# Optimization experiments

Measured on AMD Instinct MI355X. Metric: run time of the kernel, lower is better.

The kernel has to match this reference:

```python
import jax, jax.numpy as jnp
import numpy as np

# nuScenes-style config: 6 cams, 4 FPN levels of a 256x704 image
SPATIAL = np.array([[64, 176], [32, 88], [16, 44], [8, 22]], dtype=np.int32)  # (H, W) per level
NUM_CAMS = 6
EMBED = 256      # embed dims C
GROUPS = 8       # attention groups, C % GROUPS == 0
BS = 2
ANCHORS = 900    # queries
PTS = 13         # key points per anchor


def setup_inputs() -> dict:
    key = jax.random.key(0)
    k1, k2, k3 = jax.random.split(key, 3)
    hw = SPATIAL.prod(axis=1)                                   # per-level H*W
    starts = np.concatenate([[0], np.cumsum(hw)[:-1]]).astype(np.int32)
    num_value = NUM_CAMS * int(hw.sum())                        # 6 * 14960 = 89760
    value = jax.random.normal(k1, (BS, num_value, EMBED), jnp.float32)
    input_spatial_shapes = jnp.asarray(np.tile(SPATIAL[None], (NUM_CAMS, 1, 1)))   # [cams, lvls, 2]
    input_level_start_index = jnp.asarray(np.tile(starts[None], (NUM_CAMS, 1)))    # [cams, lvls]
    sampling_locations = jax.random.uniform(k2, (BS, ANCHORS, PTS, NUM_CAMS, 2), jnp.float32)
    attention_weights = jax.random.uniform(k3, (BS, ANCHORS, PTS, NUM_CAMS, SPATIAL.shape[0], GROUPS), jnp.float32)
    return {
        "value": value,
        "input_spatial_shapes": input_spatial_shapes,
        "input_level_start_index": input_level_start_index,
        "sampling_locations": sampling_locations,
        "attention_weights": attention_weights,
    }


def _dfa(value, shapes, starts, loc, weights):
    """Multi-scale multi-camera deformable aggregation (Sparse4D kernel math)."""
    bs, num_value, c = value.shape
    num_cams, num_levels = shapes.shape[:2]
    _, A, P = loc.shape[:3]
    groups = weights.shape[-1]
    gdim = c // groups
    per_cam = num_value // num_cams
    value_c = value.reshape(bs, num_cams, per_cam, c)           # cam-major layout
    b_idx = jnp.arange(bs)[:, None, None, None]
    cam_idx = jnp.arange(num_cams)[None, None, None, :]
    loc_w = loc[..., 0]                                          # [bs, A, P, cams]
    loc_h = loc[..., 1]
    out = jnp.zeros((bs, A, groups, gdim), value.dtype)
    for lvl in range(num_levels):                                # static small loop over levels
        H = int(shapes[0, lvl, 0]); W = int(shapes[0, lvl, 1]); s = int(starts[0, lvl])
        featf = value_c[:, :, s:s + H * W, :]                    # [bs, cams, H*W, c]
        h = loc_h * H - 0.5
        w = loc_w * W - 0.5
        h0 = jnp.floor(h); w0 = jnp.floor(w)
        dh = h - h0; dw = w - w0
        h0i = h0.astype(jnp.int32); w0i = w0.astype(jnp.int32)

        def corner(hi, wi, bw):
            valid = (hi >= 0) & (hi < H) & (wi >= 0) & (wi < W)  # zero padding outside
            idx = jnp.clip(hi, 0, H - 1) * W + jnp.clip(wi, 0, W - 1)
            v = featf[b_idx, cam_idx, idx]                       # gather -> [bs, A, P, cams, c]
            return v * (bw * valid)[..., None]

        samp = (corner(h0i,     w0i,     (1 - dh) * (1 - dw))
              + corner(h0i,     w0i + 1, (1 - dh) * dw)
              + corner(h0i + 1, w0i,     dh * (1 - dw))
              + corner(h0i + 1, w0i + 1, dh * dw))               # bilinear sample [bs, A, P, cams, c]
        samp = samp.reshape(bs, A, P, num_cams, groups, gdim)
        out = out + jnp.einsum("bapcgd,bapcg->bagd", samp, weights[..., lvl, :])
    return out.reshape(bs, A, c)


def reference(value, input_spatial_shapes, input_level_start_index, sampling_locations, attention_weights):
    shapes = np.asarray(input_spatial_shapes)
    starts = np.asarray(input_level_start_index)
    return _dfa(value, shapes, starts, sampling_locations, attention_weights)
```

## Files before the change

kernel.cpp:

```cpp
#include <hip/hip_runtime.h>

constexpr int NCAMS   = 6;
constexpr int EMB     = 256;
constexpr int NGROUPS = 8;
constexpr int NLVL    = 4;
constexpr int NPTS    = 13;
constexpr int NPAIR   = NPTS * NCAMS;

__global__ __launch_bounds__(256, 4)
void dfa_kernel(const float* __restrict__ value,
                const int*   __restrict__ shapes,
                const int*   __restrict__ starts,
                const float* __restrict__ loc,
                const float* __restrict__ attw,
                float*       __restrict__ out,
                int A, int per_cam)
{
    const int tid  = threadIdx.x;
    const int wv   = tid >> 6;
    const int lane = tid & 63;
    const int b = blockIdx.x / A;
    const int a = blockIdx.x - b * A;

    __shared__ int   sH[NLVL], sW[NLVL], sS[NLVL];
    __shared__ float red[4][EMB];
    if (tid < NLVL) {
        sH[tid] = shapes[tid * 2 + 0];
        sW[tid] = shapes[tid * 2 + 1];
        sS[tid] = starts[tid];
    }
    __syncthreads();

    const int g = lane >> 3;
    const long ba = (long)b * A + a;
    const float* locp = loc  + ba * (NPTS * NCAMS * 2);
    const float* awp  = attw + ba * (NPTS * NCAMS * NLVL * NGROUPS) + g;

    float4 acc = make_float4(0.f, 0.f, 0.f, 0.f);

    for (int pair = wv; pair < NPAIR; pair += 4) {
        const int p = pair / NCAMS;
        const int c = pair - p * NCAMS;
        const float lw = locp[pair * 2 + 0];
        const float lh = locp[pair * 2 + 1];
        const float* vb = value + ((long)(b * NCAMS + c) * per_cam) * EMB + lane * 4;
        const float* awpc = awp + pair * (NLVL * NGROUPS);

        #pragma unroll
        for (int lvl = 0; lvl < NLVL; ++lvl) {
            const int H = sH[lvl], W = sW[lvl], S = sS[lvl];
            const float hf = lh * (float)H - 0.5f;
            const float wf = lw * (float)W - 0.5f;
            const float h0f = floorf(hf), w0f = floorf(wf);
            const float dh = hf - h0f, dw = wf - w0f;
            const int h0 = (int)h0f, w0 = (int)w0f;
            const int h1 = h0 + 1,  w1 = w0 + 1;

            const float aw = awpc[lvl * NGROUPS];

            float w00 = (1.f - dh) * (1.f - dw) * aw;
            float w01 = (1.f - dh) * dw         * aw;
            float w10 = dh         * (1.f - dw) * aw;
            float w11 = dh         * dw         * aw;

            const bool vh0 = (unsigned)h0 < (unsigned)H;
            const bool vh1 = (unsigned)h1 < (unsigned)H;
            const bool vw0 = (unsigned)w0 < (unsigned)W;
            const bool vw1 = (unsigned)w1 < (unsigned)W;
            w00 = (vh0 && vw0) ? w00 : 0.f;
            w01 = (vh0 && vw1) ? w01 : 0.f;
            w10 = (vh1 && vw0) ? w10 : 0.f;
            w11 = (vh1 && vw1) ? w11 : 0.f;

            const int h0c = min(max(h0, 0), H - 1);
            const int h1c = min(max(h1, 0), H - 1);
            const int w0c = min(max(w0, 0), W - 1);
            const int w1c = min(max(w1, 0), W - 1);

            const float* r0 = vb + (long)(S + h0c * W) * EMB;
            const float* r1 = vb + (long)(S + h1c * W) * EMB;

            const float4 v00 = *(const float4*)(r0 + (long)w0c * EMB);
            const float4 v01 = *(const float4*)(r0 + (long)w1c * EMB);
            const float4 v10 = *(const float4*)(r1 + (long)w0c * EMB);
            const float4 v11 = *(const float4*)(r1 + (long)w1c * EMB);

            acc.x += v00.x * w00 + v01.x * w01 + v10.x * w10 + v11.x * w11;
            acc.y += v00.y * w00 + v01.y * w01 + v10.y * w10 + v11.y * w11;
            acc.z += v00.z * w00 + v01.z * w01 + v10.z * w10 + v11.z * w11;
            acc.w += v00.w * w00 + v01.w * w01 + v10.w * w10 + v11.w * w11;
        }
    }

    *(float4*)&red[wv][lane * 4] = acc;
    __syncthreads();

    const float o = red[0][tid] + red[1][tid] + red[2][tid] + red[3][tid];
    out[ba * EMB + tid] = o;
}

extern "C" void kernel_launch(void* const* d_in, const int* in_sizes, int n_in,
                              void* d_out, int out_size, void* d_ws, size_t ws_size,
                              hipStream_t stream) {
    const float* value  = (const float*)d_in[0];
    const int*   shapes = (const int*)d_in[1];
    const int*   starts = (const int*)d_in[2];
    const float* loc    = (const float*)d_in[3];
    const float* attw   = (const float*)d_in[4];
    float*       out    = (float*)d_out;

    const int B = 2;
    const int A = out_size / (EMB * B);
    const int per_cam = in_sizes[0] / (B * EMB * NCAMS);

    dim3 grid(B * A);
    dim3 block(256);
    dfa_kernel<<<grid, block, 0, stream>>>(value, shapes, starts, loc, attw, out,
                                           A, per_cam);
}
```

Measured before the change: 466.5 us.

## Split per-anchor sampling pairs across extra grid dimension with partial-sum reduction

Splits each anchor's point-camera pairs across four blocks along a new grid dimension. The partial sums are written to workspace and combined by a separate reduction kernel, with an atomic fallback when workspace is too small. The aim is more independent blocks and outstanding gathers, and less tail imbalance from the long per-wave loop. In exchange it adds an extra kernel launch, workspace traffic and repeated per-block setup.

```diff
diff --git a/kernel.cpp b/kernel.cpp
--- a/kernel.cpp
+++ b/kernel.cpp
@@ -6,19 +6,22 @@
 constexpr int NLVL    = 4;
 constexpr int NPTS    = 13;
 constexpr int NPAIR   = NPTS * NCAMS;
+constexpr int SPLIT   = 4;
 
+template <bool USE_ATOMIC>
 __global__ __launch_bounds__(256, 4)
 void dfa_kernel(const float* __restrict__ value,
                 const int*   __restrict__ shapes,
                 const int*   __restrict__ starts,
                 const float* __restrict__ loc,
                 const float* __restrict__ attw,
-                float*       __restrict__ out,
+                float*       __restrict__ dst,
                 int A, int per_cam)
 {
-    const int tid  = threadIdx.x;
-    const int wv   = tid >> 6;
-    const int lane = tid & 63;
+    const int tid   = threadIdx.x;
+    const int wv    = tid >> 6;
+    const int lane  = tid & 63;
+    const int split = blockIdx.y;
     const int b = blockIdx.x / A;
     const int a = blockIdx.x - b * A;
 
@@ -38,7 +41,7 @@
 
     float4 acc = make_float4(0.f, 0.f, 0.f, 0.f);
 
-    for (int pair = wv; pair < NPAIR; pair += 4) {
+    for (int pair = wv + (split << 2); pair < NPAIR; pair += 4 * SPLIT) {
         const int p = pair / NCAMS;
         const int c = pair - p * NCAMS;
         const float lw = locp[pair * 2 + 0];
@@ -96,7 +99,32 @@
     __syncthreads();
 
     const float o = red[0][tid] + red[1][tid] + red[2][tid] + red[3][tid];
-    out[ba * EMB + tid] = o;
+    if (USE_ATOMIC) {
+        atomicAdd(&dst[ba * EMB + tid], o);
+    } else {
+        dst[((long)split * gridDim.x + ba) * EMB + tid] = o;
+    }
+}
+
+__global__ __launch_bounds__(256, 4)
+void reduce_kernel(const float* __restrict__ ws, float* __restrict__ out, int n4)
+{
+    const int i = blockIdx.x * blockDim.x + threadIdx.x;
+    if (i >= n4) return;
+    const float4* p = (const float4*)ws;
+    float4 s = p[i];
+    #pragma unroll
+    for (int sp = 1; sp < SPLIT; ++sp) {
+        const float4 q = p[(long)sp * n4 + i];
+        s.x += q.x; s.y += q.y; s.z += q.z; s.w += q.w;
+    }
+    ((float4*)out)[i] = s;
+}
+
+__global__ void zero_kernel(float* __restrict__ out, int n4)
+{
+    const int i = blockIdx.x * blockDim.x + threadIdx.x;
+    if (i < n4) ((float4*)out)[i] = make_float4(0.f, 0.f, 0.f, 0.f);
 }
 
 extern "C" void kernel_launch(void* const* d_in, const int* in_sizes, int n_in,
@@ -112,9 +140,22 @@
     const int B = 2;
     const int A = out_size / (EMB * B);
     const int per_cam = in_sizes[0] / (B * EMB * NCAMS);
+    const int BA = B * A;
+    const size_t need = (size_t)SPLIT * BA * EMB * sizeof(float);
 
-    dim3 grid(B * A);
+    dim3 grid(BA, SPLIT);
     dim3 block(256);
-    dfa_kernel<<<grid, block, 0, stream>>>(value, shapes, starts, loc, attw, out,
-                                           A, per_cam);
+
+    if (ws_size >= need) {
+        float* ws = (float*)d_ws;
+        dfa_kernel<false><<<grid, block, 0, stream>>>(value, shapes, starts, loc,
+                                                      attw, ws, A, per_cam);
+        const int n4 = BA * EMB / 4;
+        reduce_kernel<<<(n4 + 255) / 256, 256, 0, stream>>>(ws, out, n4);
+    } else {
+        const int n4 = BA * EMB / 4;
+        zero_kernel<<<(n4 + 255) / 256, 256, 0, stream>>>(out, n4);
+        dfa_kernel<true><<<grid, block, 0, stream>>>(value, shapes, starts, loc,
+                                                     attw, out, A, per_cam);
+    }
 }
```

Result: faster. 449.5 us (-3.6%).
